# Optimization experiments

Hardware: AMD Instinct MI355X
Metric: run time of the kernel (lower is better)

## Reference

```python
import jax, jax.numpy as jnp
import numpy as np

N, E, D, H, C, ED = 10000, 160000, 128, 4, 128, 1
NEG_SLOPE = 0.2
LN_EPS = 1e-5
SM_EPS = 1e-16


def setup_inputs() -> dict:
    key = jax.random.key(0)
    ks = jax.random.split(key, 12)
    s = 0.05  # weight scale (glorot-ish, keeps attention logits tame)
    return {
        "x": jax.random.normal(ks[0], (N, D), jnp.float32),
        "edge_index": jax.random.randint(ks[1], (2, E), 0, N, jnp.int64),
        "edge_attr": jax.random.uniform(ks[2], (E, ED), jnp.float32),
        "Wl": jax.random.normal(ks[3], (D, H * C), jnp.float32) * s,
        "bl": jnp.zeros((H * C,), jnp.float32),
        "Wr": jax.random.normal(ks[4], (D, H * C), jnp.float32) * s,
        "br": jnp.zeros((H * C,), jnp.float32),
        "We": jax.random.normal(ks[5], (ED, H * C), jnp.float32) * s,
        "att": jax.random.normal(ks[6], (1, H, C), jnp.float32) * s,
        "bias_out": jnp.zeros((H * C,), jnp.float32),
        "Wp": jax.random.normal(ks[7], (H * C, D), jnp.float32) * s,
        "bp": jnp.zeros((D,), jnp.float32),
        "gamma": jnp.ones((D,), jnp.float32),
        "beta": jnp.zeros((D,), jnp.float32),
    }


def _gat_block(x, edge_index, edge_attr, Wl, bl, Wr, br, We, att, bias_out, Wp, bp, gamma, beta):
    n, d = x.shape
    h, c = att.shape[1], att.shape[2]
    src, dst = edge_index[0], edge_index[1]
    # add_self_loops=True; fill_value='mean' for edge_attr of self loops
    loop = jnp.arange(n)
    src = jnp.concatenate([src, loop])
    dst = jnp.concatenate([dst, loop])
    ea_mean = edge_attr.mean(axis=0, keepdims=True)
    ea = jnp.concatenate([edge_attr, jnp.broadcast_to(ea_mean, (n, edge_attr.shape[1]))], axis=0)
    # GATv2: x_l, x_r linear transforms -> [N, H, C]
    xl = (x @ Wl + bl).reshape(n, h, c)
    xr = (x @ Wr + br).reshape(n, h, c)
    e = (ea @ We).reshape(-1, h, c)
    # per-edge attention logits: leaky_relu(x_j + x_i + e) . att
    z = xl[src] + xr[dst] + e                      # [E', H, C]
    z = jnp.where(z > 0, z, NEG_SLOPE * z)
    alpha = jnp.einsum('ehc,hc->eh', z, att[0])    # [E', H]
    # segment softmax over incoming edges of each destination node
    m = jax.ops.segment_max(alpha, dst, num_segments=n)
    alpha = jnp.exp(alpha - m[dst])
    ssum = jax.ops.segment_sum(alpha, dst, num_segments=n)
    alpha = alpha / (ssum[dst] + SM_EPS)
    # weighted scatter-add of source messages x_l[src]
    out = jax.ops.segment_sum(alpha[:, :, None] * xl[src], dst, num_segments=n)
    hcat = out.reshape(n, h * c) + bias_out
    # dense epilogue: proj + residual + gelu + layernorm (dropout = eval identity)
    y = hcat @ Wp + bp
    y = y + x  # residual (in_dim == out_dim)
    y = jax.nn.gelu(y, approximate=False)
    mu = y.mean(-1, keepdims=True)
    var = ((y - mu) ** 2).mean(-1, keepdims=True)
    y = (y - mu) / jnp.sqrt(var + LN_EPS) * gamma + beta
    return y


def reference(x, edge_index, edge_attr, Wl, bl, Wr, br, We, att, bias_out, Wp, bp, gamma, beta):
    return _gat_block(x, edge_index, edge_attr, Wl, bl, Wr, br, We, att, bias_out, Wp, bp, gamma, beta)
```

## Files before the change

### kernel.cpp

```cpp
#include <hip/hip_runtime.h>
#include <hip/hip_bf16.h>

#define NN 10000
#define NE 160000
#define DD 128
#define HC 512
#define SEG 96
#define POISON 0xAAAAAAAAu

typedef __bf16 bf16x8 __attribute__((ext_vector_type(8)));
typedef float f32x4 __attribute__((ext_vector_type(4)));

__device__ __forceinline__ unsigned short f2bs(float f) {
    __hip_bfloat16 h = __float2bfloat16(f);
    return *(unsigned short*)&h;
}

__global__ __launch_bounds__(256) void k_init(const float* __restrict__ Wl,
                                              const float* __restrict__ Wr,
                                              const float* __restrict__ Wp,
                                              const float* __restrict__ ea,
                                              unsigned short* __restrict__ WbT,
                                              unsigned short* __restrict__ WpT,
                                              float* __restrict__ eapart) {
    __shared__ float ws4[4];
    int t = threadIdx.x;
    int i = blockIdx.x * 256 + t;
    int stride = gridDim.x * 256;
    for (int idx = i; idx < 1024 * DD; idx += stride) {
        int n = idx >> 7, k = idx & 127;
        float v = (n < 512) ? Wl[k * HC + n] : Wr[k * HC + (n - 512)];
        WbT[idx] = f2bs(v);
    }
    for (int idx = i; idx < 128 * 512; idx += stride) {
        int n = idx >> 9, k = idx & 511;
        WpT[idx] = f2bs(Wp[k * DD + n]);
    }
    if (blockIdx.x < 64) {
        int b0 = blockIdx.x * 2500;
        float v = 0.f;
        for (int j = b0 + t; j < b0 + 2500; j += 256) v += ea[j];
        for (int off = 32; off >= 1; off >>= 1) v += __shfl_xor(v, off);
        if ((t & 63) == 0) ws4[t >> 6] = v;
        __syncthreads();
        if (t == 0) eapart[blockIdx.x] = ws4[0] + ws4[1] + ws4[2] + ws4[3];
    }
}

#define GM 64
#define GN 128
#define LDA 136
#define LDB 136
#define MTILES 157
#define GEMM_BLOCKS (MTILES * 8)
#define SCAT_BLOCKS 625

__global__ __launch_bounds__(256) void k_big(const float* __restrict__ x,
                                             const unsigned short* __restrict__ WbT,
                                             const float* __restrict__ bl,
                                             const float* __restrict__ br,
                                             unsigned short* __restrict__ xlrb,
                                             const int* __restrict__ ei,
                                             const float* __restrict__ ea,
                                             int* __restrict__ cnt2,
                                             int2* __restrict__ sorted2) {
    __shared__ __attribute__((aligned(16))) unsigned short As[GM * LDA];
    __shared__ __attribute__((aligned(16))) unsigned short Bs[GN * LDB];
    int t = threadIdx.x;
    int blk = blockIdx.x;
    if (blk >= GEMM_BLOCKS) {
        int e = (blk - GEMM_BLOCKS) * 256 + t;
        int d = ei[NE + e];
        unsigned old = atomicAdd((unsigned*)&cnt2[d], 1u);
        int pos = d * SEG + (int)(old - POISON);
        sorted2[pos] = make_int2(ei[e], __float_as_int(ea[e]));
        return;
    }
    int mb = blk % MTILES, nb = blk / MTILES;
    for (int i = t; i < GM * 32; i += 256) {
        int r = i >> 5, c4 = i & 31;
        int row = mb * GM + r;
        float4 v = (row < NN) ? *(const float4*)(x + (size_t)row * DD + c4 * 4)
                              : make_float4(0.f, 0.f, 0.f, 0.f);
        ushort4 u;
        u.x = f2bs(v.x); u.y = f2bs(v.y); u.z = f2bs(v.z); u.w = f2bs(v.w);
        *(ushort4*)(As + r * LDA + c4 * 4) = u;
    }
    const uint4* gB = (const uint4*)(WbT + (size_t)nb * GN * DD);
    for (int i = t; i < GN * 16; i += 256) {
        int r = i >> 4, c = i & 15;
        ((uint4*)(Bs + r * LDB))[c] = gB[i];
    }
    __syncthreads();
    int wave = t >> 6, lane = t & 63;
    int l15 = lane & 15, quad = lane >> 4;
    f32x4 acc[4][2];
#pragma unroll
    for (int rf = 0; rf < 4; ++rf)
#pragma unroll
        for (int cf = 0; cf < 2; ++cf) acc[rf][cf] = (f32x4){0.f, 0.f, 0.f, 0.f};
#pragma unroll
    for (int ks = 0; ks < 4; ++ks) {
        int k0 = ks * 32 + quad * 8;
        bf16x8 af[4];
#pragma unroll
        for (int rf = 0; rf < 4; ++rf)
            af[rf] = *(const bf16x8*)(As + (rf * 16 + l15) * LDA + k0);
#pragma unroll
        for (int cf = 0; cf < 2; ++cf) {
            int nloc = wave * 32 + cf * 16 + l15;
            bf16x8 b = *(const bf16x8*)(Bs + nloc * LDB + k0);
#pragma unroll
            for (int rf = 0; rf < 4; ++rf)
                acc[rf][cf] = __builtin_amdgcn_mfma_f32_16x16x32_bf16(af[rf], b, acc[rf][cf], 0, 0, 0);
        }
    }
    int nbase = nb * GN + wave * 32;
#pragma unroll
    for (int rf = 0; rf < 4; ++rf) {
#pragma unroll
        for (int cf = 0; cf < 2; ++cf) {
            int nn = nbase + cf * 16 + l15;
            float bv = (nn < 512) ? bl[nn] : br[nn - 512];
#pragma unroll
            for (int reg = 0; reg < 4; ++reg) {
                int m = mb * GM + rf * 16 + quad * 4 + reg;
                if (m < NN) xlrb[(size_t)m * 1024 + nn] = f2bs(acc[rf][cf][reg] + bv);
            }
        }
    }
}

__global__ __launch_bounds__(256) void k_attn(const unsigned short* __restrict__ xlrb,
                                              const float* __restrict__ We,
                                              const float* __restrict__ att,
                                              const float* __restrict__ bias_out,
                                              const int* __restrict__ cnt2,
                                              const int2* __restrict__ sorted2,
                                              const float* __restrict__ eapart,
                                              unsigned short* __restrict__ hcatb) {
    int t = threadIdx.x;
    int wave = t >> 6, lane = t & 63;
    int n = blockIdx.x * 4 + wave;
    int li = lane & 15;
    int h = lane >> 4;
    int base = h * 128 + li * 8;

    float eamean;
    {
        float v = eapart[lane];
        for (int off = 32; off >= 1; off >>= 1) v += __shfl_xor(v, off);
        eamean = v * (1.0f / NE);
    }

    float att8[8], We8[8], xr8[8], bo8[8];
    *(float4*)&att8[0] = *(const float4*)&att[base];
    *(float4*)&att8[4] = *(const float4*)&att[base + 4];
    *(float4*)&We8[0]  = *(const float4*)&We[base];
    *(float4*)&We8[4]  = *(const float4*)&We[base + 4];
    *(float4*)&bo8[0]  = *(const float4*)&bias_out[base];
    *(float4*)&bo8[4]  = *(const float4*)&bias_out[base + 4];
    {
        uint4 u = *(const uint4*)(xlrb + (size_t)n * 1024 + 512 + base);
        xr8[0] = __uint_as_float(u.x << 16); xr8[1] = __uint_as_float(u.x & 0xffff0000u);
        xr8[2] = __uint_as_float(u.y << 16); xr8[3] = __uint_as_float(u.y & 0xffff0000u);
        xr8[4] = __uint_as_float(u.z << 16); xr8[5] = __uint_as_float(u.z & 0xffff0000u);
        xr8[6] = __uint_as_float(u.w << 16); xr8[7] = __uint_as_float(u.w & 0xffff0000u);
    }

    int count = (int)((unsigned)cnt2[n] - POISON);
    count = (count < 0) ? 0 : ((count > SEG) ? SEG : count);
    const int2* seg = sorted2 + (size_t)n * SEG;

    float p, acc8[8];
    {
        uint4 u = *(const uint4*)(xlrb + (size_t)n * 1024 + base);
        float x8[8];
        x8[0] = __uint_as_float(u.x << 16); x8[1] = __uint_as_float(u.x & 0xffff0000u);
        x8[2] = __uint_as_float(u.y << 16); x8[3] = __uint_as_float(u.y & 0xffff0000u);
        x8[4] = __uint_as_float(u.z << 16); x8[5] = __uint_as_float(u.z & 0xffff0000u);
        x8[6] = __uint_as_float(u.w << 16); x8[7] = __uint_as_float(u.w & 0xffff0000u);
        float d = 0.f;
#pragma unroll
        for (int i = 0; i < 8; ++i) {
            float z = fmaf(eamean, We8[i], xr8[i]) + x8[i];
            float l = fmaf(0.2f, fminf(z, 0.f), fmaxf(z, 0.f));
            d = fmaf(l, att8[i], d);
        }
#pragma unroll
        for (int off = 8; off >= 1; off >>= 1) d += __shfl_xor(d, off);
        float w = __expf(d);
        p = w;
#pragma unroll
        for (int i = 0; i < 8; ++i) acc8[i] = w * x8[i];
    }

    int pos = 0;
    bool have = pos < count;
    int2 se;
    uint4 nx;
    if (have) {
        se = seg[pos];
        nx = *(const uint4*)(xlrb + (size_t)se.x * 1024 + base);
    }
    while (have) {
        uint4 cx = nx;
        float eav = __int_as_float(se.y);
        int npos = pos + 1;
        bool nhave = npos < count;
        if (nhave) {
            se = seg[npos];
            nx = *(const uint4*)(xlrb + (size_t)se.x * 1024 + base);
        }
        float x8[8];
        x8[0] = __uint_as_float(cx.x << 16); x8[1] = __uint_as_float(cx.x & 0xffff0000u);
        x8[2] = __uint_as_float(cx.y << 16); x8[3] = __uint_as_float(cx.y & 0xffff0000u);
        x8[4] = __uint_as_float(cx.z << 16); x8[5] = __uint_as_float(cx.z & 0xffff0000u);
        x8[6] = __uint_as_float(cx.w << 16); x8[7] = __uint_as_float(cx.w & 0xffff0000u);
        float d = 0.f;
#pragma unroll
        for (int i = 0; i < 8; ++i) {
            float z = fmaf(eav, We8[i], xr8[i]) + x8[i];
            float l = fmaf(0.2f, fminf(z, 0.f), fmaxf(z, 0.f));
            d = fmaf(l, att8[i], d);
        }
#pragma unroll
        for (int off = 8; off >= 1; off >>= 1) d += __shfl_xor(d, off);
        float w = __expf(d);
        p += w;
#pragma unroll
        for (int i = 0; i < 8; ++i) acc8[i] = fmaf(w, x8[i], acc8[i]);
        pos = npos;
        have = nhave;
    }
    float inv = 1.0f / (p + 1e-16f);
    unsigned short o8[8];
#pragma unroll
    for (int i = 0; i < 8; ++i) o8[i] = f2bs(fmaf(acc8[i], inv, bo8[i]));
    *(uint4*)(hcatb + (size_t)n * HC + base) = *(uint4*)o8;
}

#define OGM 32
__global__ __launch_bounds__(256) void k_out2(const unsigned short* __restrict__ hcatb,
                                              const unsigned short* __restrict__ WpT,
                                              const float* __restrict__ bp,
                                              const float* __restrict__ x,
                                              const float* __restrict__ gamma,
                                              const float* __restrict__ beta,
                                              float* __restrict__ out) {
    __shared__ __attribute__((aligned(16))) unsigned short As[OGM * LDA];
    __shared__ __attribute__((aligned(16))) unsigned short Bs[GN * LDB];
    __shared__ float ys[OGM * DD];
    int t = threadIdx.x;
    int n0 = blockIdx.x * OGM;
    int wave = t >> 6, lane = t & 63;
    int l15 = lane & 15, quad = lane >> 4;
    f32x4 acc[2][2];
#pragma unroll
    for (int rf = 0; rf < 2; ++rf)
#pragma unroll
        for (int cf = 0; cf < 2; ++cf) acc[rf][cf] = (f32x4){0.f, 0.f, 0.f, 0.f};

    for (int kc = 0; kc < 4; ++kc) {
        for (int i = t; i < OGM * 16; i += 256) {
            int r = i >> 4, c = i & 15;
            int row = n0 + r;
            uint4 v = (row < NN)
                ? *(const uint4*)(hcatb + (size_t)row * HC + kc * 128 + c * 8)
                : make_uint4(0u, 0u, 0u, 0u);
            *(uint4*)(As + r * LDA + c * 8) = v;
        }
        for (int i = t; i < GN * 16; i += 256) {
            int r = i >> 4, c = i & 15;
            *(uint4*)(Bs + r * LDB + c * 8) =
                *(const uint4*)(WpT + (size_t)r * HC + kc * 128 + c * 8);
        }
        __syncthreads();
        const unsigned short* aB0 = As + l15 * LDA;
        const unsigned short* aB1 = As + (16 + l15) * LDA;
#pragma unroll
        for (int ks = 0; ks < 4; ++ks) {
            int k0 = ks * 32 + quad * 8;
            bf16x8 a0 = *(const bf16x8*)(aB0 + k0);
            bf16x8 a1 = *(const bf16x8*)(aB1 + k0);
#pragma unroll
            for (int cf = 0; cf < 2; ++cf) {
                int nloc = wave * 32 + cf * 16 + l15;
                bf16x8 b = *(const bf16x8*)(Bs + nloc * LDB + k0);
                acc[0][cf] = __builtin_amdgcn_mfma_f32_16x16x32_bf16(a0, b, acc[0][cf], 0, 0, 0);
                acc[1][cf] = __builtin_amdgcn_mfma_f32_16x16x32_bf16(a1, b, acc[1][cf], 0, 0, 0);
            }
        }
        __syncthreads();
    }
#pragma unroll
    for (int rf = 0; rf < 2; ++rf) {
#pragma unroll
        for (int cf = 0; cf < 2; ++cf) {
            int nn = wave * 32 + cf * 16 + l15;
            float bv = bp[nn];
#pragma unroll
            for (int reg = 0; reg < 4; ++reg) {
                int mloc = rf * 16 + quad * 4 + reg;
                int row = n0 + mloc;
                float y = acc[rf][cf][reg] + bv;
                if (row < NN) y += x[(size_t)row * DD + nn];
                y = 0.5f * y * (1.f + erff(y * 0.70710678118f));
                ys[mloc * DD + nn] = y;
            }
        }
    }
    __syncthreads();
#pragma unroll
    for (int i = 0; i < 8; ++i) {
        int r = wave * 8 + i;
        int row = n0 + r;
        float v0 = ys[r * DD + lane];
        float v1 = ys[r * DD + 64 + lane];
        float s = v0 + v1, q = v0 * v0 + v1 * v1;
        for (int off = 32; off >= 1; off >>= 1) {
            s += __shfl_xor(s, off);
            q += __shfl_xor(q, off);
        }
        float mu = s * (1.f / 128.f);
        float var = q * (1.f / 128.f) - mu * mu;
        float inv = rsqrtf(fmaxf(var, 0.f) + 1e-5f);
        if (row < NN) {
            out[(size_t)row * DD + lane] = (v0 - mu) * inv * gamma[lane] + beta[lane];
            out[(size_t)row * DD + 64 + lane] = (v1 - mu) * inv * gamma[64 + lane] + beta[64 + lane];
        }
    }
}

#define ALIGN16(p) ((char*)(((uintptr_t)(p) + 15) & ~(uintptr_t)15))

extern "C" void kernel_launch(void* const* d_in, const int* in_sizes, int n_in,
                              void* d_out, int out_size, void* d_ws, size_t ws_size,
                              hipStream_t stream) {
    const float* x        = (const float*)d_in[0];
    const int*   ei       = (const int*)d_in[1];
    const float* ea       = (const float*)d_in[2];
    const float* Wl       = (const float*)d_in[3];
    const float* bl       = (const float*)d_in[4];
    const float* Wr       = (const float*)d_in[5];
    const float* br       = (const float*)d_in[6];
    const float* We       = (const float*)d_in[7];
    const float* att      = (const float*)d_in[8];
    const float* bias_out = (const float*)d_in[9];
    const float* Wp       = (const float*)d_in[10];
    const float* bp       = (const float*)d_in[11];
    const float* gamma    = (const float*)d_in[12];
    const float* beta     = (const float*)d_in[13];
    float* out = (float*)d_out;

    char* p = (char*)d_ws;
    unsigned short* xlrb  = (unsigned short*)p; p += (size_t)(MTILES * GM) * 1024 * 2;
    unsigned short* hcatb = (unsigned short*)p; p += (size_t)(MTILES * GM) * HC * 2;
    unsigned short* WbT   = (unsigned short*)p; p += (size_t)1024 * DD * 2;
    unsigned short* WpT   = (unsigned short*)p; p += (size_t)128 * HC * 2;
    float* eapart  = (float*)p;  p += 64 * 4;
    int*   cnt2    = (int*)p;    p += NN * 4;
    p = ALIGN16(p);
    int2*  sorted2 = (int2*)p;   p += (size_t)NN * SEG * 8;

    k_init<<<128, 256, 0, stream>>>(Wl, Wr, Wp, ea, WbT, WpT, eapart);
    k_big<<<GEMM_BLOCKS + SCAT_BLOCKS, 256, 0, stream>>>(
        x, WbT, bl, br, xlrb, ei, ea, cnt2, sorted2);
    k_attn<<<NN / 4, 256, 0, stream>>>(xlrb, We, att, bias_out, cnt2, sorted2, eapart, hcatb);
    k_out2<<<(NN + OGM - 1) / OGM, 256, 0, stream>>>(hcatb, WpT, bp, x, gamma, beta, out);
}
```

Baseline: 167.6 us.

## Deepen edge gather prefetch to four in flight and cache segment indices via shuffles

Replaces the one-ahead prefetch in the per-node aggregation loop with a four-deep software pipeline that keeps four source-row gathers in flight, unrolled four ways. Each lane also loads one entry of the node's edge list once, and the first 64 entries are broadcast with shuffles instead of being reloaded from memory. The aim is to hide gather latency on the random xl rows. The cost is higher register pressure and possibly lower occupancy.

```diff
diff --git a/kernel.cpp b/kernel.cpp
--- a/kernel.cpp
+++ b/kernel.cpp
@@ -172,6 +172,12 @@
     count = (count < 0) ? 0 : ((count > SEG) ? SEG : count);
     const int2* seg = sorted2 + (size_t)n * SEG;
 
+    int2 myse = seg[lane];
+    auto get_se = [&](int idx) -> int2 {
+        if (idx < 64) return make_int2(__shfl(myse.x, idx), __shfl(myse.y, idx));
+        return seg[idx];
+    };
+
     float p, acc8[8];
     {
         uint4 u = *(const uint4*)(xlrb + (size_t)n * 1024 + base);
@@ -195,44 +201,67 @@
         for (int i = 0; i < 8; ++i) acc8[i] = w * x8[i];
     }
 
+    uint4 xb0, xb1, xb2, xb3;
+    float ev0, ev1, ev2, ev3;
+#define PRELOAD(J)                                                          \
+    if (J < count) {                                                        \
+        int2 se_ = get_se(J);                                               \
+        ev##J = __int_as_float(se_.y);                                      \
+        xb##J = *(const uint4*)(xlrb + (size_t)se_.x * 1024 + base);        \
+    }
+    PRELOAD(0) PRELOAD(1) PRELOAD(2) PRELOAD(3)
+#undef PRELOAD
+
+#define COMPUTE(CX, EV)                                                     \
+    {                                                                       \
+        float x8[8];                                                        \
+        x8[0] = __uint_as_float(CX.x << 16);                                \
+        x8[1] = __uint_as_float(CX.x & 0xffff0000u);                        \
+        x8[2] = __uint_as_float(CX.y << 16);                                \
+        x8[3] = __uint_as_float(CX.y & 0xffff0000u);                        \
+        x8[4] = __uint_as_float(CX.z << 16);                                \
+        x8[5] = __uint_as_float(CX.z & 0xffff0000u);                        \
+        x8[6] = __uint_as_float(CX.w << 16);                                \
+        x8[7] = __uint_as_float(CX.w & 0xffff0000u);                        \
+        float d = 0.f;                                                      \
+        _Pragma("unroll") for (int i = 0; i < 8; ++i) {                     \
+            float z = fmaf(EV, We8[i], xr8[i]) + x8[i];                     \
+            float l = fmaf(0.2f, fminf(z, 0.f), fmaxf(z, 0.f));             \
+            d = fmaf(l, att8[i], d);                                        \
+        }                                                                   \
+        _Pragma("unroll") for (int off = 8; off >= 1; off >>= 1)            \
+            d += __shfl_xor(d, off);                                        \
+        float w = __expf(d);                                                \
+        p += w;                                                             \
+        _Pragma("unroll") for (int i = 0; i < 8; ++i)                       \
+            acc8[i] = fmaf(w, x8[i], acc8[i]);                              \
+    }
+
+#define STEP(J)                                                             \
+    {                                                                       \
+        uint4 cx_ = xb##J;                                                  \
+        float ev_ = ev##J;                                                  \
+        int np_ = pos + J + 4;                                              \
+        if (np_ < count) {                                                  \
+            int2 se_ = get_se(np_);                                         \
+            ev##J = __int_as_float(se_.y);                                  \
+            xb##J = *(const uint4*)(xlrb + (size_t)se_.x * 1024 + base);    \
+        }                                                                   \
+        COMPUTE(cx_, ev_)                                                   \
+    }
+
     int pos = 0;
-    bool have = pos < count;
-    int2 se;
-    uint4 nx;
-    if (have) {
-        se = seg[pos];
-        nx = *(const uint4*)(xlrb + (size_t)se.x * 1024 + base);
-    }
-    while (have) {
-        uint4 cx = nx;
-        float eav = __int_as_float(se.y);
-        int npos = pos + 1;
-        bool nhave = npos < count;
-        if (nhave) {
-            se = seg[npos];
-            nx = *(const uint4*)(xlrb + (size_t)se.x * 1024 + base);
-        }
-        float x8[8];
-        x8[0] = __uint_as_float(cx.x << 16); x8[1] = __uint_as_float(cx.x & 0xffff0000u);
-        x8[2] = __uint_as_float(cx.y << 16); x8[3] = __uint_as_float(cx.y & 0xffff0000u);
-        x8[4] = __uint_as_float(cx.z << 16); x8[5] = __uint_as_float(cx.z & 0xffff0000u);
-        x8[6] = __uint_as_float(cx.w << 16); x8[7] = __uint_as_float(cx.w & 0xffff0000u);
-        float d = 0.f;
-#pragma unroll
-        for (int i = 0; i < 8; ++i) {
-            float z = fmaf(eav, We8[i], xr8[i]) + x8[i];
-            float l = fmaf(0.2f, fminf(z, 0.f), fmaxf(z, 0.f));
-            d = fmaf(l, att8[i], d);
-        }
-#pragma unroll
-        for (int off = 8; off >= 1; off >>= 1) d += __shfl_xor(d, off);
-        float w = __expf(d);
-        p += w;
-#pragma unroll
-        for (int i = 0; i < 8; ++i) acc8[i] = fmaf(w, x8[i], acc8[i]);
-        pos = npos;
-        have = nhave;
-    }
+    while (pos + 4 <= count) {
+        STEP(0) STEP(1) STEP(2) STEP(3)
+        pos += 4;
+    }
+    if (pos + 0 < count) COMPUTE(xb0, ev0)
+    if (pos + 1 < count) COMPUTE(xb1, ev1)
+    if (pos + 2 < count) COMPUTE(xb2, ev2)
+    if (pos + 3 < count) COMPUTE(xb3, ev3)
+#undef STEP
+#undef COMPUTE
+
     float inv = 1.0f / (p + 1e-16f);
     unsigned short o8[8];
 #pragma unroll
```

Measured after the change: 166.1 us. Within noise of the previous version (-0.9%).
